# Kernel optimization log

Hardware: AMD Instinct MI355X
Metric: run time of the kernel (lower is better)

The kernel has to match this reference:

```python
import jax, jax.numpy as jnp
import numpy as np

N_HEAD = 16
ROPE_BASE = 10000.0

def rotate_half(x):
    half = x.shape[-1] // 2
    return jnp.concatenate((-x[..., half:], x[..., :half]), axis=-1)

def rope_freqs(T, head_dim, dtype):
    inv_freq = 1.0 / (ROPE_BASE ** (jnp.arange(0, head_dim, 2, dtype=jnp.float32) / head_dim))
    t = jnp.arange(T, dtype=jnp.float32)
    freqs = t[:, None] * inv_freq[None, :]          # [T, head_dim//2]
    emb = jnp.concatenate((freqs, freqs), axis=-1)  # [T, head_dim]
    return emb.astype(dtype)

def setup_inputs() -> dict:
    key = jax.random.key(0)
    ks = jax.random.split(key, 9)
    B, T, C = 2, 2048, 1024
    s = 1.0 / np.sqrt(C)
    return {
        'x':  jax.random.normal(ks[0], (B, T, C), jnp.float32),
        'Wq': jax.random.normal(ks[1], (C, C), jnp.float32) * s,
        'bq': jnp.zeros((C,), jnp.float32),
        'Wk': jax.random.normal(ks[2], (C, C), jnp.float32) * s,
        'bk': jnp.zeros((C,), jnp.float32),
        'Wv': jax.random.normal(ks[3], (C, C), jnp.float32) * s,
        'bv': jnp.zeros((C,), jnp.float32),
        'Wp': jax.random.normal(ks[4], (C, C), jnp.float32) * s,
        'bp': jnp.zeros((C,), jnp.float32),
    }

def reference(x, Wq, bq, Wk, bk, Wv, bv, Wp, bp):
    B, T, C = x.shape
    H = N_HEAD
    D = C // H
    # torch Linear: y = x @ W.T + b
    def heads(y):
        return y.reshape(B, T, H, D).transpose(0, 2, 1, 3)  # [B,H,T,D]
    q = heads(x @ Wq.T + bq)
    k = heads(x @ Wk.T + bk)
    v = heads(x @ Wv.T + bv)
    # inline RoPE
    emb = rope_freqs(T, D, x.dtype)          # [T, D]
    cos, sin = jnp.cos(emb), jnp.sin(emb)
    q = q * cos + rotate_half(q) * sin
    k = k * cos + rotate_half(k) * sin
    # full T x T scores with causal masked softmax
    att = jnp.einsum('bhtd,bhsd->bhts', q, k) * (1.0 / jnp.sqrt(jnp.array(D, x.dtype)))
    causal = jnp.tril(jnp.ones((T, T), bool))
    att = jnp.where(causal[None, None], att, jnp.array(-jnp.inf, att.dtype))
    att = jax.nn.softmax(att, axis=-1)
    y = jnp.einsum('bhts,bhsd->bhtd', att, v)  # [B,H,T,D]
    y = y.transpose(0, 2, 1, 3).reshape(B, T, C)
    return y @ Wp.T + bp
```

## Files before the change

### kernel.cpp

```cpp
#include <hip/hip_runtime.h>
#include <hip/hip_bf16.h>
#include <stdint.h>

typedef unsigned short u16;
typedef __attribute__((ext_vector_type(8))) short bf16x8;
typedef __attribute__((ext_vector_type(4))) float f32x4;
typedef __attribute__((ext_vector_type(2))) unsigned int u32x2;

typedef const __attribute__((address_space(1))) unsigned int* gu32p;
typedef __attribute__((address_space(3))) unsigned int* lu32p;

__device__ __forceinline__ void gl_lds16(const u16* g, u16* l) {
  __builtin_amdgcn_global_load_lds((gu32p)(const void*)g, (lu32p)(void*)l, 16, 0, 0);
}

__device__ __forceinline__ u16 f2bf(float f) {
  union { float f; unsigned u; } v; v.f = f;
  unsigned r = v.u + 0x7fffu + ((v.u >> 16) & 1u);
  return (u16)(r >> 16);
}
__device__ __forceinline__ void st2bf(u16* p0, u16* p1, float a, float b) {
  union { __hip_bfloat162 h; u16 u[2]; } cv;
  cv.h = __float22bfloat162_rn(make_float2(a, b));
  *p0 = cv.u[0]; *p1 = cv.u[1];
}
__device__ __forceinline__ unsigned pk2bf(float a, float b) {
  union { __hip_bfloat162 h; unsigned u; } cv;
  cv.h = __float22bfloat162_rn(make_float2(a, b));
  return cv.u;
}

__global__ void convert_kernel(const float4* __restrict__ x, const float4* __restrict__ wq,
                               const float4* __restrict__ wk, const float4* __restrict__ wv,
                               const float4* __restrict__ wp,
                               u16* __restrict__ xb, u16* __restrict__ wqb, u16* __restrict__ wkb,
                               u16* __restrict__ wvb, u16* __restrict__ wpb,
                               float2* __restrict__ tab) {
  int i = blockIdx.x * 256 + threadIdx.x;
  const int NX = 1048576, NW = 262144, NCONV = NX + 4 * NW;
  if (i >= NCONV) {
    int j = i - NCONV;
    int d = j & 31, t = j >> 5;
    float ang = (float)t * expf(-0.28782313662425572f * (float)d);
    tab[j] = make_float2(cosf(ang), sinf(ang));
    return;
  }
  const float4* src; u16* dst; int off;
  if (i < NX)            { src = x;  dst = xb;  off = i; }
  else if (i < NX + NW)  { src = wq; dst = wqb; off = i - NX; }
  else if (i < NX + 2*NW){ src = wk; dst = wkb; off = i - NX - NW; }
  else if (i < NX + 3*NW){ src = wv; dst = wvb; off = i - NX - 2*NW; }
  else                   { src = wp; dst = wpb; off = i - NX - 3*NW; }
  float4 v = src[off];
  ushort4 ov = make_ushort4(f2bf(v.x), f2bf(v.y), f2bf(v.z), f2bf(v.w));
  *(ushort4*)&dst[off * 4] = ov;
}

template<int FUSE_ROPE, int OUT_BF16, int TRANS_V>
__global__ __launch_bounds__(256) void gemm_bt_kernel(
    const u16* __restrict__ A,
    const u16* __restrict__ B0, const u16* __restrict__ B1, const u16* __restrict__ B2,
    const float* __restrict__ bias0, const float* __restrict__ bias1, const float* __restrict__ bias2,
    void* out0, void* out1, void* out2, const float2* __restrict__ tab)
{
  __shared__ __align__(16) u16 As[2][4096];
  __shared__ __align__(16) u16 Bs[2][4096];
  const int z = blockIdx.z;
  const u16* Bw = (z == 0) ? B0 : (z == 1) ? B1 : B2;
  const float* bias = (z == 0) ? bias0 : (z == 1) ? bias1 : bias2;
  void* outv = (z == 0) ? out0 : (z == 1) ? out1 : out2;
  const int tid = threadIdx.x, lane = tid & 63, w = tid >> 6;
  const int wr = w >> 1, wc = w & 1;
  const int quad = lane >> 4, l15 = lane & 15;
  const int m0 = blockIdx.y * 128, n0 = blockIdx.x * 128;
  const int sr = lane >> 2, sc = (lane & 3) * 8;

  auto stg = [&](int kt, int bf) {
    const int k0 = kt * 32;
    #pragma unroll
    for (int p = 0; p < 2; p++) {
      gl_lds16(A  + (m0 + p*64 + w*16 + sr) * 1024 + k0 + sc, &As[bf][p*2048 + w*512]);
      gl_lds16(Bw + (n0 + p*64 + w*16 + sr) * 1024 + k0 + sc, &Bs[bf][p*2048 + w*512]);
    }
  };

  f32x4 acc[4][4] = {};
  stg(0, 0);
  for (int kt = 0; kt < 32; kt++) {
    __syncthreads();
    if (kt < 31) stg(kt + 1, (kt + 1) & 1);
    const int bf = kt & 1;
    bf16x8 af[4], bfr[4];
    #pragma unroll
    for (int mt = 0; mt < 4; mt++)
      af[mt] = *(const bf16x8*)&As[bf][(wr*64 + mt*16 + l15) * 32 + quad*8];
    #pragma unroll
    for (int nt = 0; nt < 4; nt++)
      bfr[nt] = *(const bf16x8*)&Bs[bf][(wc*64 + nt*16 + l15) * 32 + quad*8];
    #pragma unroll
    for (int mt = 0; mt < 4; mt++)
      #pragma unroll
      for (int nt = 0; nt < 4; nt++)
        acc[mt][nt] = __builtin_amdgcn_mfma_f32_16x16x32_bf16(af[mt], bfr[nt], acc[mt][nt], 0, 0, 0);
  }

  if (TRANS_V && z == 2) {
    const int bb = m0 >> 11, tg0 = (m0 & 2047) + wr*64 + quad*4;
    #pragma unroll
    for (int nt = 0; nt < 4; nt++) {
      const int c = n0 + wc*64 + nt*16 + l15;
      const float bv = bias[c];
      u16* vrow = (u16*)outv + (size_t)(bb*1024 + c) * 2048 + tg0;
      #pragma unroll
      for (int mt = 0; mt < 4; mt++) {
        ushort4 pk;
        pk.x = f2bf(acc[mt][nt][0] + bv); pk.y = f2bf(acc[mt][nt][1] + bv);
        pk.z = f2bf(acc[mt][nt][2] + bv); pk.w = f2bf(acc[mt][nt][3] + bv);
        *(ushort4*)&vrow[mt*16] = pk;
      }
    }
    return;
  }

  #pragma unroll
  for (int mt = 0; mt < 4; mt++) {
    #pragma unroll
    for (int r = 0; r < 4; r++) {
      const int row = m0 + wr*64 + mt*16 + quad*4 + r;
      float v[4];
      #pragma unroll
      for (int nt = 0; nt < 4; nt++)
        v[nt] = acc[mt][nt][r] + bias[n0 + wc*64 + nt*16 + l15];
      if (FUSE_ROPE && z < 2) {
        const int t = row & 2047;
        #pragma unroll
        for (int nt = 0; nt < 2; nt++) {
          const int d = nt*16 + l15;
          float2 cs = tab[t*32 + d];
          float x0 = v[nt], x1 = v[nt+2];
          v[nt]   = x0 * cs.x - x1 * cs.y;
          v[nt+2] = x1 * cs.x + x0 * cs.y;
        }
      }
      #pragma unroll
      for (int nt = 0; nt < 4; nt++) {
        const int col = n0 + wc*64 + nt*16 + l15;
        if (OUT_BF16) ((u16*)outv)[row * 1024 + col] = f2bf(v[nt]);
        else          ((float*)outv)[row * 1024 + col] = v[nt];
      }
    }
  }
}

__global__ __launch_bounds__(512) void attn_kernel(
    const u16* __restrict__ qg, const u16* __restrict__ kg,
    const u16* __restrict__ vtg, u16* __restrict__ yg)
{
  __shared__ __align__(16) u16 K_lds[2][128 * 64];
  __shared__ __align__(16) u16 V_lds[2][64 * 128];
  const int x = blockIdx.x;
  const int hh = blockIdx.y, b = blockIdx.z;
  const int tid = threadIdx.x, lane = tid & 63, w = tid >> 6;
  const int wt = w >> 2;
  const int quad = lane >> 4, l15 = lane & 15;
  const int bh = b * (2048 * 1024) + hh * 64;
  const int vtb = (b * 16 + hh) * 131072;

  const int qtA = x, qtB = 15 - x;
  const int qt_w = wt ? qtB : qtA;
  const int wl = w & 3;

  bf16x8 qf[2][2];
  #pragma unroll
  for (int rg = 0; rg < 2; rg++) {
    const int qrow = qt_w*128 + rg*64 + wl*16 + l15;
    qf[rg][0] = *(const bf16x8*)&qg[bh + qrow*1024 + quad*8];
    qf[rg][1] = *(const bf16x8*)&qg[bh + qrow*1024 + 32 + quad*8];
  }
  f32x4 o[2][4] = {};
  f32x4 l5[2] = {};

  bf16x8 ones;
  #pragma unroll
  for (int i2 = 0; i2 < 8; i2++) ones[i2] = (short)0x3F80;

  const float c = 0.18033688011112042f;

  auto do_stage = [&](int j, int bf) {
    #pragma unroll
    for (int p = 0; p < 2; p++) {
      const int seg = w*2 + p;
      const int r = seg*8 + (lane >> 3);
      const int g = (lane & 7) ^ (r & 7);
      gl_lds16(kg + bh + (j*128 + r) * 1024 + g*8, &K_lds[bf][seg*512]);
    }
    #pragma unroll
    for (int p = 0; p < 2; p++) {
      const int seg = w*2 + p;
      const int r = seg*4 + (lane >> 4);
      const int g = (lane & 15) ^ (r & 15);
      gl_lds16(vtg + vtb + r * 2048 + j*128 + g*8, &V_lds[bf][seg*512]);
    }
  };

  do_stage(0, 0);
  for (int j = 0; j <= qtB; j++) {
    __syncthreads();
    if (j < qtB) do_stage(j + 1, (j + 1) & 1);
    const int bf = j & 1;
    if (wt == 0 && j > qtA) continue;
    const bool diag = (j == qt_w);

    #pragma unroll
    for (int ss = 0; ss < 4; ss++) {
      f32x4 s[2][2];
      #pragma unroll
      for (int h = 0; h < 2; h++) {
        const int nt = ss*2 + h;
        const int krow = (nt*16 + l15) * 64;
        const int g0 = ((quad)     ^ (l15 & 7)) * 8;
        const int g1 = ((4 + quad) ^ (l15 & 7)) * 8;
        bf16x8 kf0 = *(const bf16x8*)&K_lds[bf][krow + g0];
        bf16x8 kf1 = *(const bf16x8*)&K_lds[bf][krow + g1];
        #pragma unroll
        for (int rg = 0; rg < 2; rg++) {
          f32x4 z = {};
          z = __builtin_amdgcn_mfma_f32_16x16x32_bf16(kf0, qf[rg][0], z, 0, 0, 0);
          z = __builtin_amdgcn_mfma_f32_16x16x32_bf16(kf1, qf[rg][1], z, 0, 0, 0);
          s[rg][h] = z;
        }
      }
      if (diag) {
        #pragma unroll
        for (int rg = 0; rg < 2; rg++) {
          const int qrow = rg*64 + wl*16 + l15;
          #pragma unroll
          for (int h = 0; h < 2; h++)
            #pragma unroll
            for (int r = 0; r < 4; r++)
              if ((ss*2 + h)*16 + quad*4 + r > qrow) s[rg][h][r] = -1e30f;
        }
      }
      bf16x8 pa[2];
      #pragma unroll
      for (int rg = 0; rg < 2; rg++) {
        float a0 = exp2f(s[rg][0][0] * c), a1 = exp2f(s[rg][0][1] * c);
        float a2 = exp2f(s[rg][0][2] * c), a3 = exp2f(s[rg][0][3] * c);
        float b0 = exp2f(s[rg][1][0] * c), b1 = exp2f(s[rg][1][1] * c);
        float b2 = exp2f(s[rg][1][2] * c), b3 = exp2f(s[rg][1][3] * c);
        unsigned A01 = pk2bf(a0, a1), A23 = pk2bf(a2, a3);
        unsigned B01 = pk2bf(b0, b1), B23 = pk2bf(b2, b3);
        u32x2 t0 = __builtin_amdgcn_permlane32_swap(A01, B01, false, false);
        u32x2 w02 = __builtin_amdgcn_permlane16_swap(t0[0], t0[1], false, false);
        u32x2 t1 = __builtin_amdgcn_permlane32_swap(A23, B23, false, false);
        u32x2 w13 = __builtin_amdgcn_permlane16_swap(t1[0], t1[1], false, false);
        union { unsigned u[4]; bf16x8 v; } pk;
        pk.u[0] = w02[0]; pk.u[1] = w13[0]; pk.u[2] = w02[1]; pk.u[3] = w13[1];
        pa[rg] = pk.v;
      }
      l5[0] = __builtin_amdgcn_mfma_f32_16x16x32_bf16(pa[0], ones, l5[0], 0, 0, 0);
      l5[1] = __builtin_amdgcn_mfma_f32_16x16x32_bf16(pa[1], ones, l5[1], 0, 0, 0);
      #pragma unroll
      for (int dt = 0; dt < 4; dt++) {
        const int vg = ((ss*4 + quad) ^ l15) * 8;
        bf16x8 vf = *(const bf16x8*)&V_lds[bf][(dt*16 + l15)*128 + vg];
        o[0][dt] = __builtin_amdgcn_mfma_f32_16x16x32_bf16(pa[0], vf, o[0][dt], 0, 0, 0);
        o[1][dt] = __builtin_amdgcn_mfma_f32_16x16x32_bf16(pa[1], vf, o[1][dt], 0, 0, 0);
      }
    }
  }

  #pragma unroll
  for (int rg = 0; rg < 2; rg++)
    #pragma unroll
    for (int r = 0; r < 4; r++) {
      float inv = 1.0f / l5[rg][r];
      u16* yr = &yg[bh + (qt_w*128 + rg*64 + wl*16 + quad*4 + r) * 1024 + l15];
      st2bf(yr,      yr + 16, o[rg][0][r] * inv, o[rg][1][r] * inv);
      st2bf(yr + 32, yr + 48, o[rg][2][r] * inv, o[rg][3][r] * inv);
    }
}

extern "C" void kernel_launch(void* const* d_in, const int* in_sizes, int n_in,
                              void* d_out, int out_size, void* d_ws, size_t ws_size,
                              hipStream_t stream) {
  const float* x  = (const float*)d_in[0];
  const float* Wq = (const float*)d_in[1];
  const float* bq = (const float*)d_in[2];
  const float* Wk = (const float*)d_in[3];
  const float* bk = (const float*)d_in[4];
  const float* Wv = (const float*)d_in[5];
  const float* bv = (const float*)d_in[6];
  const float* Wp = (const float*)d_in[7];
  const float* bp = (const float*)d_in[8];

  char* ws = (char*)d_ws;
  u16* xb  = (u16*)(ws);
  u16* wqb = (u16*)(ws + (8u  << 20));
  u16* wkb = (u16*)(ws + (10u << 20));
  u16* wvb = (u16*)(ws + (12u << 20));
  u16* wpb = (u16*)(ws + (14u << 20));
  u16* qb  = (u16*)(ws + (16u << 20));
  u16* kb  = (u16*)(ws + (24u << 20));
  u16* vtb = (u16*)(ws + (32u << 20));
  float2* tab = (float2*)(ws + (40u << 20));
  u16* yb = xb;

  convert_kernel<<<8448, 256, 0, stream>>>((const float4*)x, (const float4*)Wq, (const float4*)Wk,
                                           (const float4*)Wv, (const float4*)Wp,
                                           xb, wqb, wkb, wvb, wpb, tab);
  gemm_bt_kernel<1, 1, 1><<<dim3(8, 32, 3), 256, 0, stream>>>(xb, wqb, wkb, wvb, bq, bk, bv,
                                                              (void*)qb, (void*)kb, (void*)vtb, tab);
  attn_kernel<<<dim3(8, 16, 2), 512, 0, stream>>>(qb, kb, vtb, yb);
  gemm_bt_kernel<0, 0, 0><<<dim3(8, 32, 1), 256, 0, stream>>>(yb, wpb, wpb, wpb, bp, bp, bp,
                                                              (void*)d_out, (void*)d_out, (void*)d_out, tab);
}
```

Measured before the change: 210.7 us.

## Split attention into one q-tile per 256-thread block and prescale Q

The attention kernel used to pair two causal q-tiles (x and 15-x) inside a 512-thread block, with half the warps idle once their shorter tile finished. Now each 256-thread block handles a single q-tile over a 16x16x2 grid. Batch 0 takes the tiles in reverse order so long and short blocks interleave. The softmax scale and log2e factor move into the Q projection epilogue, and the exp uses the raw hardware exp2 builtin, which drops a multiply per score. Each block now loads K/V for only one tile, so there is less reuse per load, and the long diagonal blocks may leave a load-imbalance tail.

```diff
diff --git a/kernel.cpp b/kernel.cpp
--- a/kernel.cpp
+++ b/kernel.cpp
@@ -141,6 +141,11 @@
           v[nt]   = x0 * cs.x - x1 * cs.y;
           v[nt+2] = x1 * cs.x + x0 * cs.y;
         }
+        if (z == 0) {
+          const float SC = 0.18033688011112042f;
+          #pragma unroll
+          for (int nt = 0; nt < 4; nt++) v[nt] *= SC;
+        }
       }
       #pragma unroll
       for (int nt = 0; nt < 4; nt++) {
@@ -152,7 +157,7 @@
   }
 }
 
-__global__ __launch_bounds__(512) void attn_kernel(
+__global__ __launch_bounds__(256) void attn_kernel(
     const u16* __restrict__ qg, const u16* __restrict__ kg,
     const u16* __restrict__ vtg, u16* __restrict__ yg)
 {
@@ -160,20 +165,16 @@
   __shared__ __align__(16) u16 V_lds[2][64 * 128];
   const int x = blockIdx.x;
   const int hh = blockIdx.y, b = blockIdx.z;
+  const int qt = b ? x : (15 - x);
   const int tid = threadIdx.x, lane = tid & 63, w = tid >> 6;
-  const int wt = w >> 2;
   const int quad = lane >> 4, l15 = lane & 15;
   const int bh = b * (2048 * 1024) + hh * 64;
   const int vtb = (b * 16 + hh) * 131072;
 
-  const int qtA = x, qtB = 15 - x;
-  const int qt_w = wt ? qtB : qtA;
-  const int wl = w & 3;
-
   bf16x8 qf[2][2];
   #pragma unroll
   for (int rg = 0; rg < 2; rg++) {
-    const int qrow = qt_w*128 + rg*64 + wl*16 + l15;
+    const int qrow = qt*128 + rg*64 + w*16 + l15;
     qf[rg][0] = *(const bf16x8*)&qg[bh + qrow*1024 + quad*8];
     qf[rg][1] = *(const bf16x8*)&qg[bh + qrow*1024 + 32 + quad*8];
   }
@@ -184,19 +185,17 @@
   #pragma unroll
   for (int i2 = 0; i2 < 8; i2++) ones[i2] = (short)0x3F80;
 
-  const float c = 0.18033688011112042f;
-
   auto do_stage = [&](int j, int bf) {
     #pragma unroll
-    for (int p = 0; p < 2; p++) {
-      const int seg = w*2 + p;
+    for (int p = 0; p < 4; p++) {
+      const int seg = w*4 + p;
       const int r = seg*8 + (lane >> 3);
       const int g = (lane & 7) ^ (r & 7);
       gl_lds16(kg + bh + (j*128 + r) * 1024 + g*8, &K_lds[bf][seg*512]);
     }
     #pragma unroll
-    for (int p = 0; p < 2; p++) {
-      const int seg = w*2 + p;
+    for (int p = 0; p < 4; p++) {
+      const int seg = w*4 + p;
       const int r = seg*4 + (lane >> 4);
       const int g = (lane & 15) ^ (r & 15);
       gl_lds16(vtg + vtb + r * 2048 + j*128 + g*8, &V_lds[bf][seg*512]);
@@ -204,12 +203,11 @@
   };
 
   do_stage(0, 0);
-  for (int j = 0; j <= qtB; j++) {
+  for (int j = 0; j <= qt; j++) {
     __syncthreads();
-    if (j < qtB) do_stage(j + 1, (j + 1) & 1);
+    if (j < qt) do_stage(j + 1, (j + 1) & 1);
     const int bf = j & 1;
-    if (wt == 0 && j > qtA) continue;
-    const bool diag = (j == qt_w);
+    const bool diag = (j == qt);
 
     #pragma unroll
     for (int ss = 0; ss < 4; ss++) {
@@ -233,7 +231,7 @@
       if (diag) {
         #pragma unroll
         for (int rg = 0; rg < 2; rg++) {
-          const int qrow = rg*64 + wl*16 + l15;
+          const int qrow = rg*64 + w*16 + l15;
           #pragma unroll
           for (int h = 0; h < 2; h++)
             #pragma unroll
@@ -244,10 +242,10 @@
       bf16x8 pa[2];
       #pragma unroll
       for (int rg = 0; rg < 2; rg++) {
-        float a0 = exp2f(s[rg][0][0] * c), a1 = exp2f(s[rg][0][1] * c);
-        float a2 = exp2f(s[rg][0][2] * c), a3 = exp2f(s[rg][0][3] * c);
-        float b0 = exp2f(s[rg][1][0] * c), b1 = exp2f(s[rg][1][1] * c);
-        float b2 = exp2f(s[rg][1][2] * c), b3 = exp2f(s[rg][1][3] * c);
+        float a0 = __builtin_amdgcn_exp2f(s[rg][0][0]), a1 = __builtin_amdgcn_exp2f(s[rg][0][1]);
+        float a2 = __builtin_amdgcn_exp2f(s[rg][0][2]), a3 = __builtin_amdgcn_exp2f(s[rg][0][3]);
+        float b0 = __builtin_amdgcn_exp2f(s[rg][1][0]), b1 = __builtin_amdgcn_exp2f(s[rg][1][1]);
+        float b2 = __builtin_amdgcn_exp2f(s[rg][1][2]), b3 = __builtin_amdgcn_exp2f(s[rg][1][3]);
         unsigned A01 = pk2bf(a0, a1), A23 = pk2bf(a2, a3);
         unsigned B01 = pk2bf(b0, b1), B23 = pk2bf(b2, b3);
         u32x2 t0 = __builtin_amdgcn_permlane32_swap(A01, B01, false, false);
@@ -275,7 +273,7 @@
     #pragma unroll
     for (int r = 0; r < 4; r++) {
       float inv = 1.0f / l5[rg][r];
-      u16* yr = &yg[bh + (qt_w*128 + rg*64 + wl*16 + quad*4 + r) * 1024 + l15];
+      u16* yr = &yg[bh + (qt*128 + rg*64 + w*16 + quad*4 + r) * 1024 + l15];
       st2bf(yr,      yr + 16, o[rg][0][r] * inv, o[rg][1][r] * inv);
       st2bf(yr + 32, yr + 48, o[rg][2][r] * inv, o[rg][3][r] * inv);
     }
@@ -311,7 +309,7 @@
                                            xb, wqb, wkb, wvb, wpb, tab);
   gemm_bt_kernel<1, 1, 1><<<dim3(8, 32, 3), 256, 0, stream>>>(xb, wqb, wkb, wvb, bq, bk, bv,
                                                               (void*)qb, (void*)kb, (void*)vtb, tab);
-  attn_kernel<<<dim3(8, 16, 2), 512, 0, stream>>>(qb, kb, vtb, yb);
+  attn_kernel<<<dim3(16, 16, 2), 256, 0, stream>>>(qb, kb, vtb, yb);
   gemm_bt_kernel<0, 0, 0><<<dim3(8, 32, 1), 256, 0, stream>>>(yb, wpb, wpb, wpb, bp, bp, bp,
                                                               (void*)d_out, (void*)d_out, (void*)d_out, tab);
 }
```

Result: faster. 197.5 us (-6.2%).
